# Optimization experiments

Hardware: AMD Instinct MI355X
Metric: run time of the kernel (lower is better)

The kernel has to match this reference:

```python
import jax, jax.numpy as jnp
from jax import lax
import numpy as np

O = 64      # out_channels (== in_channels == groups, depthwise)
P = 3       # prompt_len
K = 17      # prompt_size (large kernel size)
RANK = 4
# (small_kernel_size, pixel_unshuffle_scale, dilations) for prompt_size=17
CONFIGS = [(3, 4, (4, 5, 7)), (5, 2, (1,)), (9, 1, (2,))]


def conv2d(x, w, b=None, stride=1, padding=0, dilation=1, groups=1):
    out = lax.conv_general_dilated(
        x, w, (stride, stride), [(padding, padding)] * 2,
        rhs_dilation=(dilation, dilation), feature_group_count=groups,
        dimension_numbers=('NCHW', 'OIHW', 'NCHW'))
    return out if b is None else out + b[None, :, None, None]


def pixel_unshuffle(x, s):
    n, c, h, w = x.shape
    x = x.reshape(n, c, h // s, s, w // s, s)
    return x.transpose(0, 1, 3, 5, 2, 4).reshape(n, c * s * s, h // s, w // s)


def bilinear(x, oh, ow):
    # F.interpolate(mode='bilinear', align_corners=False); all uses downsample
    n, c, h, w = x.shape
    def coords(o, i):
        src = jnp.clip((jnp.arange(o, dtype=jnp.float32) + 0.5) * (i / o) - 0.5, 0.0, i - 1.0)
        i0 = jnp.floor(src).astype(jnp.int32)
        i1 = jnp.minimum(i0 + 1, i - 1)
        return i0, i1, src - i0.astype(jnp.float32)
    y0, y1, ty = coords(oh, h)
    x0, x1, tx = coords(ow, w)
    r0, r1 = x[:, :, y0], x[:, :, y1]
    top = r0[:, :, :, x0] * (1 - tx) + r0[:, :, :, x1] * tx
    bot = r1[:, :, :, x0] * (1 - tx) + r1[:, :, :, x1] * tx
    ty = ty[:, None]
    return top * (1 - ty) + bot * ty


def zero_interleave(k, d):
    # conv_transpose2d with 1x1 ones kernel, stride d == insert d-1 zeros
    o, c, ks, _ = k.shape
    e = d * (ks - 1) + 1
    return jnp.zeros((o, c, e, e), k.dtype).at[:, :, ::d, ::d].set(k)


def _branch(weight0, k_size, scale, dils, dw_w, dw_b, w1, b1, w2, b2, dilw, merged):
    w = weight0
    if scale > 1:
        ph = (-K) % scale
        w = jnp.pad(w, ((0, 0), (0, 0), (0, ph), (0, ph)))
        w = pixel_unshuffle(w, scale)
    h = conv2d(w, dw_w, dw_b, padding=1, groups=dw_w.shape[0])  # depthwise 3x3
    h = jax.nn.relu(conv2d(h, w1, b1))                          # 1x1 expand
    h = conv2d(h, w2, b2)                                       # 1x1 project
    h = bilinear(h, k_size, k_size)                             # (O, P*scale_or_P, k, k)
    for idx, d in enumerate(dils):
        dk = jnp.einsum('ochw,pc->ophw', h, dilw[idx])          # 1x1, no bias -> (O,P,k,k)
        eq = zero_interleave(dk, d)
        p = K // 2 - eq.shape[-1] // 2
        merged = merged + jnp.pad(eq, ((0, 0), (0, 0), (p, p), (p, p)))
    return merged


def _forward(x, A1, A2, A3, B1, B2, B3,
             dw_w3, dw_b3, w1_3, b1_3, w2_3, b2_3, dilw3,
             dw_w5, dw_b5, w1_5, b1_5, w2_5, b2_5, dilw5,
             dw_w9, dw_b9, w1_9, b1_9, w2_9, b2_9, dilw9):
    # low-rank reconstruction: (O,1,K,r) @ (O,1,r,K) -> (O,1,K,K), cat -> (O,P,K,K)
    weight0 = jnp.concatenate(
        [jnp.einsum('oikj,oijl->oikl', A, B) for A, B in ((A1, B1), (A2, B2), (A3, B3))],
        axis=1)
    merged = jnp.zeros_like(weight0)
    packs = [(dw_w3, dw_b3, w1_3, b1_3, w2_3, b2_3, dilw3),
             (dw_w5, dw_b5, w1_5, b1_5, w2_5, b2_5, dilw5),
             (dw_w9, dw_b9, w1_9, b1_9, w2_9, b2_9, dilw9)]
    for (k_size, scale, dils), pk in zip(CONFIGS, packs):
        merged = _branch(weight0, k_size, scale, dils, *pk, merged)
    w = merged.reshape(O * P, 1, K, K)
    return conv2d(x, w, padding=K // 2, groups=64)  # depthwise, 3 filters per channel


def setup_inputs() -> dict:
    key = jax.random.key(0)
    ks = iter(jax.random.split(key, 64))
    def rn(shape, s=0.05):
        return jax.random.normal(next(ks), shape, jnp.float32) * s
    inp = {'x': jax.random.normal(next(ks), (8, 64, 256, 256), jnp.float32)}
    for i in (1, 2, 3):
        inp[f'A{i}'] = rn((O, 1, K, RANK), 0.2)
        inp[f'B{i}'] = rn((O, 1, RANK, K), 0.2)
    # (pixel_unshuffle channels, hidden, mlp_out, n_dilations) per kernel size
    specs = {3: (48, 64, 12, 3), 5: (12, 48, 6, 1), 9: (3, 12, 3, 1)}
    for kk, (c, hid, out_c, nd) in specs.items():
        inp[f'dw_w{kk}'] = rn((c, 1, 3, 3))
        inp[f'dw_b{kk}'] = rn((c,))
        inp[f'w1_{kk}'] = rn((hid, c, 1, 1))
        inp[f'b1_{kk}'] = rn((hid,))
        inp[f'w2_{kk}'] = rn((out_c, hid, 1, 1))
        inp[f'b2_{kk}'] = rn((out_c,))
        inp[f'dilw{kk}'] = rn((nd, P, out_c))
    return inp


def reference(x, A1, A2, A3, B1, B2, B3,
              dw_w3, dw_b3, w1_3, b1_3, w2_3, b2_3, dilw3,
              dw_w5, dw_b5, w1_5, b1_5, w2_5, b2_5, dilw5,
              dw_w9, dw_b9, w1_9, b1_9, w2_9, b2_9, dilw9):
    return _forward(x, A1, A2, A3, B1, B2, B3,
                    dw_w3, dw_b3, w1_3, b1_3, w2_3, b2_3, dilw3,
                    dw_w5, dw_b5, w1_5, b1_5, w2_5, b2_5, dilw5,
                    dw_w9, dw_b9, w1_9, b1_9, w2_9, b2_9, dilw9)
```

## Files before the change

### kernel.cpp

```cpp
#include <hip/hip_runtime.h>
#include <cstddef>

typedef _Float16 h8 __attribute__((ext_vector_type(8)));
typedef float f4 __attribute__((ext_vector_type(4)));
typedef unsigned int uint32;

struct BranchP {
  int ksz, scale, CIN, HID, COUT, S, nd;
  int dils[3];
  const float *dw_w, *dw_b, *w1, *b1, *w2, *b2, *dilw;
};

__device__ void run_branch(int tid, const BranchP P,
                           const float* w0, float* merged,
                           float* bufA, float* bufB) {
  const int S = P.S, ksz = P.ksz, CIN = P.CIN, HID = P.HID, COUT = P.COUT;
  const int SS = S * S;
  for (int i = tid; i < CIN * SS; i += 256) {
    const int cc = i / SS, rem = i % SS, hh = rem / S, ww = rem % S;
    const int s2 = P.scale * P.scale;
    const int c = cc / s2, r2 = cc % s2, si = r2 / P.scale, sj = r2 % P.scale;
    const int sh = hh * P.scale + si, sw = ww * P.scale + sj;
    bufA[i] = (sh < 17 && sw < 17) ? w0[c * 289 + sh * 17 + sw] : 0.f;
  }
  __syncthreads();
  for (int i = tid; i < CIN * SS; i += 256) {
    const int ch = i / SS, rem = i % SS, y = rem / S, x = rem % S;
    float acc = P.dw_b[ch];
    for (int u = 0; u < 3; ++u)
      for (int v = 0; v < 3; ++v) {
        const int yy = y + u - 1, xx = x + v - 1;
        if (yy >= 0 && yy < S && xx >= 0 && xx < S)
          acc += bufA[ch * SS + yy * S + xx] * P.dw_w[ch * 9 + u * 3 + v];
      }
    bufB[i] = acc;
  }
  __syncthreads();
  for (int i = tid; i < HID * SS; i += 256) {
    const int ho = i / SS, rem = i % SS;
    float acc = P.b1[ho];
    for (int ci = 0; ci < CIN; ++ci) acc += bufB[ci * SS + rem] * P.w1[ho * CIN + ci];
    bufA[i] = fmaxf(acc, 0.f);
  }
  __syncthreads();
  for (int i = tid; i < COUT * SS; i += 256) {
    const int po = i / SS, rem = i % SS;
    float acc = P.b2[po];
    for (int ci = 0; ci < HID; ++ci) acc += bufA[ci * SS + rem] * P.w2[po * HID + ci];
    bufB[i] = acc;
  }
  __syncthreads();
  for (int i = tid; i < COUT * ksz * ksz; i += 256) {
    const int c = i / (ksz * ksz), rem = i % (ksz * ksz), oy = rem / ksz, ox = rem % ksz;
    const float ratio = (float)S / (float)ksz;
    float sy = fminf(fmaxf((oy + 0.5f) * ratio - 0.5f, 0.f), (float)(S - 1));
    float sx = fminf(fmaxf((ox + 0.5f) * ratio - 0.5f, 0.f), (float)(S - 1));
    const int y0 = (int)sy; const int y1 = min(y0 + 1, S - 1); const float ty = sy - (float)y0;
    const int x0 = (int)sx; const int x1 = min(x0 + 1, S - 1); const float tx = sx - (float)x0;
    const float* img = bufB + c * SS;
    const float top = img[y0 * S + x0] * (1.f - tx) + img[y0 * S + x1] * tx;
    const float bot = img[y1 * S + x0] * (1.f - tx) + img[y1 * S + x1] * tx;
    bufA[i] = top * (1.f - ty) + bot * ty;
  }
  __syncthreads();
  for (int di = 0; di < P.nd; ++di) {
    const int d = P.dils[di];
    const int e = d * (ksz - 1) + 1, pp = 8 - e / 2;
    for (int i = tid; i < 3 * ksz * ksz; i += 256) {
      const int p = i / (ksz * ksz), rem = i % (ksz * ksz), ih = rem / ksz, iw = rem % ksz;
      float acc = 0.f;
      for (int c2 = 0; c2 < COUT; ++c2)
        acc += bufA[c2 * ksz * ksz + rem] * P.dilw[(di * 3 + p) * COUT + c2];
      merged[p * 289 + (pp + d * ih) * 17 + (pp + d * iw)] += acc;
    }
  }
  __syncthreads();
}

#define KPAD 416
#define ACH (2 * 16 * KPAD)

__global__ __launch_bounds__(256) void prep_kernel(
    const float* __restrict__ A1, const float* __restrict__ B1,
    const float* __restrict__ A2, const float* __restrict__ B2,
    const float* __restrict__ A3, const float* __restrict__ B3,
    const float* __restrict__ dw_w3, const float* __restrict__ dw_b3,
    const float* __restrict__ w1_3, const float* __restrict__ b1_3,
    const float* __restrict__ w2_3, const float* __restrict__ b2_3,
    const float* __restrict__ dilw3,
    const float* __restrict__ dw_w5, const float* __restrict__ dw_b5,
    const float* __restrict__ w1_5, const float* __restrict__ b1_5,
    const float* __restrict__ w2_5, const float* __restrict__ b2_5,
    const float* __restrict__ dilw5,
    const float* __restrict__ dw_w9, const float* __restrict__ dw_b9,
    const float* __restrict__ w1_9, const float* __restrict__ b1_9,
    const float* __restrict__ w2_9, const float* __restrict__ b2_9,
    const float* __restrict__ dilw9,
    _Float16* __restrict__ wA) {
  const int o = blockIdx.x;
  const int tid = threadIdx.x;
  __shared__ float w0[3 * 289];
  __shared__ float merged[3 * 289];
  __shared__ float bufA[3888];
  __shared__ float bufB[3888];

  for (int i = tid; i < 3 * 289; i += 256) {
    const int c = i / 289, rem = i % 289, k = rem / 17, l = rem % 17;
    const float* A = (c == 0 ? A1 : (c == 1 ? A2 : A3)) + o * 68;
    const float* B = (c == 0 ? B1 : (c == 1 ? B2 : B3)) + o * 68;
    float s = 0.f;
    for (int r = 0; r < 4; ++r) s += A[k * 4 + r] * B[r * 17 + l];
    w0[i] = s;
    merged[i] = 0.f;
  }
  __syncthreads();

  {
    BranchP P{3, 4, 48, 64, 12, 5, 3, {4, 5, 7}, dw_w3, dw_b3, w1_3, b1_3, w2_3, b2_3, dilw3};
    run_branch(tid, P, w0, merged, bufA, bufB);
  }
  {
    BranchP P{5, 2, 12, 48, 6, 9, 1, {1, 0, 0}, dw_w5, dw_b5, w1_5, b1_5, w2_5, b2_5, dilw5};
    run_branch(tid, P, w0, merged, bufA, bufB);
  }
  {
    BranchP P{9, 1, 3, 12, 3, 17, 1, {2, 0, 0}, dw_w9, dw_b9, w1_9, b1_9, w2_9, b2_9, dilw9};
    run_branch(tid, P, w0, merged, bufA, bufB);
  }

  for (int i = tid; i < ACH; i += 256) {
    const int g = i / (16 * KPAD);
    const int m = (i / KPAD) % 16;
    const int k = i % KPAD;
    const int dxi = k / 24, r = k % 24;
    int pp, yo;
    if (g == 0) { pp = m & 1; yo = m >> 1; } else { pp = 2; yo = m; }
    const int dy = r - 8 - yo;
    float val = 0.f;
    if (!(g == 1 && m >= 8) && dy >= -8 && dy <= 8 && dxi <= 16)
      val = merged[pp * 289 + (dy + 8) * 17 + dxi];
    wA[(size_t)o * ACH + i] = (_Float16)val;
  }
}

__global__ __launch_bounds__(256) void conv_mfma_kernel(
    const float* __restrict__ xin, const _Float16* __restrict__ wA,
    float* __restrict__ out) {
  const int yg = blockIdx.x * 32;
  const int ch = blockIdx.y;
  const int n  = blockIdx.z;
  const int tid = threadIdx.x;

#define PITCH 56
  __shared__ __align__(16) _Float16 Xt[280 * PITCH];

  const float* xim = xin + ((size_t)(n * 64 + ch)) * 65536;

  const int lane = tid & 63;
  const int wv = tid >> 6;
  const int row = lane & 15;
  const int kg = lane >> 4;

  h8 a1[13], a2[13];
  {
    const _Float16* Ab = wA + (size_t)ch * ACH + row * KPAD;
    #pragma unroll
    for (int t = 0; t < 13; ++t) {
      const int k0 = t * 32 + kg * 8;
      a1[t] = __builtin_bit_cast(h8, *(const uint4*)(Ab + k0));
      a2[t] = __builtin_bit_cast(h8, *(const uint4*)(Ab + 16 * KPAD + k0));
    }
  }

  for (int i = tid; i < 6 * 280; i += 256) {
    const int rb = i / 280, c = i % 280;
    const int gx = c - 8;
    const bool cok = (gx >= 0 && gx < 256);
    float v[8];
    #pragma unroll
    for (int rr = 0; rr < 8; ++rr) {
      const int gy = yg - 8 + rb * 8 + rr;
      v[rr] = (cok && gy >= 0 && gy < 256) ? xim[gy * 256 + gx] : 0.f;
    }
    uint4 u;
    u.x = __builtin_bit_cast(uint32, __builtin_amdgcn_cvt_pkrtz(v[0], v[1]));
    u.y = __builtin_bit_cast(uint32, __builtin_amdgcn_cvt_pkrtz(v[2], v[3]));
    u.z = __builtin_bit_cast(uint32, __builtin_amdgcn_cvt_pkrtz(v[4], v[5]));
    u.w = __builtin_bit_cast(uint32, __builtin_amdgcn_cvt_pkrtz(v[6], v[7]));
    *(uint4*)&Xt[c * PITCH + rb * 8] = u;
  }
  __syncthreads();

  int boff[13];
  #pragma unroll
  for (int t = 0; t < 13; ++t) {
    const int k0 = t * 32 + kg * 8;
    const int dxi = k0 / 24, r0 = k0 - dxi * 24;
    boff[t] = (row + dxi) * PITCH + r0;
  }

  for (int pr = 0; pr < 8; ++pr) {
    const int g = pr >> 1, cp = pr & 1;
    const int j0a = (wv * 4 + cp * 2) * 16;
    const int ba = j0a * PITCH + 8 * g;
    const int bb = ba + 16 * PITCH;
    f4 c1a = {0.f, 0.f, 0.f, 0.f}, c2a = {0.f, 0.f, 0.f, 0.f};
    f4 c1b = {0.f, 0.f, 0.f, 0.f}, c2b = {0.f, 0.f, 0.f, 0.f};
    #pragma unroll
    for (int t = 0; t < 13; ++t) {
      const h8 vba = __builtin_bit_cast(h8, *(const uint4*)&Xt[ba + boff[t]]);
      const h8 vbb = __builtin_bit_cast(h8, *(const uint4*)&Xt[bb + boff[t]]);
      c1a = __builtin_amdgcn_mfma_f32_16x16x32_f16(a1[t], vba, c1a, 0, 0, 0);
      c1b = __builtin_amdgcn_mfma_f32_16x16x32_f16(a1[t], vbb, c1b, 0, 0, 0);
      c2a = __builtin_amdgcn_mfma_f32_16x16x32_f16(a2[t], vba, c2a, 0, 0, 0);
      c2b = __builtin_amdgcn_mfma_f32_16x16x32_f16(a2[t], vbb, c2b, 0, 0, 0);
    }
    const int ygg = yg + 8 * g;
    #pragma unroll
    for (int half = 0; half < 2; ++half) {
      const int gx = j0a + half * 16 + row;
      const f4 s1 = half ? c1b : c1a;
      const f4 s2 = half ? c2b : c2a;
      #pragma unroll
      for (int reg = 0; reg < 4; ++reg) {
        const int r = kg * 4 + reg;
        out[(((size_t)n * 192 + ch * 3 + (r & 1)) * 256 + (ygg + (r >> 1))) * 256 + gx] = s1[reg];
      }
      if (kg < 2) {
        #pragma unroll
        for (int reg = 0; reg < 4; ++reg) {
          const int r = kg * 4 + reg;
          out[(((size_t)n * 192 + ch * 3 + 2) * 256 + (ygg + r)) * 256 + gx] = s2[reg];
        }
      }
    }
  }
#undef PITCH
}

extern "C" void kernel_launch(void* const* d_in, const int* in_sizes, int n_in,
                              void* d_out, int out_size, void* d_ws, size_t ws_size,
                              hipStream_t stream) {
  const float* xin = (const float*)d_in[0];
  const float* A1 = (const float*)d_in[1];
  const float* B1 = (const float*)d_in[2];
  const float* A2 = (const float*)d_in[3];
  const float* B2 = (const float*)d_in[4];
  const float* A3 = (const float*)d_in[5];
  const float* B3 = (const float*)d_in[6];
  const float* dw_w3 = (const float*)d_in[7];
  const float* dw_b3 = (const float*)d_in[8];
  const float* w1_3 = (const float*)d_in[9];
  const float* b1_3 = (const float*)d_in[10];
  const float* w2_3 = (const float*)d_in[11];
  const float* b2_3 = (const float*)d_in[12];
  const float* dilw3 = (const float*)d_in[13];
  const float* dw_w5 = (const float*)d_in[14];
  const float* dw_b5 = (const float*)d_in[15];
  const float* w1_5 = (const float*)d_in[16];
  const float* b1_5 = (const float*)d_in[17];
  const float* w2_5 = (const float*)d_in[18];
  const float* b2_5 = (const float*)d_in[19];
  const float* dilw5 = (const float*)d_in[20];
  const float* dw_w9 = (const float*)d_in[21];
  const float* dw_b9 = (const float*)d_in[22];
  const float* w1_9 = (const float*)d_in[23];
  const float* b1_9 = (const float*)d_in[24];
  const float* w2_9 = (const float*)d_in[25];
  const float* b2_9 = (const float*)d_in[26];
  const float* dilw9 = (const float*)d_in[27];

  _Float16* wA = (_Float16*)d_ws;

  prep_kernel<<<64, 256, 0, stream>>>(
      A1, B1, A2, B2, A3, B3,
      dw_w3, dw_b3, w1_3, b1_3, w2_3, b2_3, dilw3,
      dw_w5, dw_b5, w1_5, b1_5, w2_5, b2_5, dilw5,
      dw_w9, dw_b9, w1_9, b1_9, w2_9, b2_9, dilw9,
      wA);

  dim3 grid(8, 64, 8);
  conv_mfma_kernel<<<grid, 256, 0, stream>>>(xin, wA, (float*)d_out);
}
```

Measured before the change: 207.5 us.

## Restructure MFMA loop to stream weights per k-step and remap blocks across XCDs

The conv kernel now keeps all 32 output accumulators (4 column tiles x 4 row groups, two weight halves) live and iterates once over the 13 k-steps, loading each weight fragment from global memory just in time with one-step prefetch instead of holding 26 weight vectors in registers. The grid is flattened to 1D with an index swizzle so that consecutive block IDs (which are dealt round-robin across XCDs) map to the same image and channel neighbourhood, improving L2 locality. A launch bound of 3 blocks per SM is added to cap register use. The risks are a larger accumulator footprint (128 VGPRs of accumulators) that could force spills under the new bound, and global weight loads now sitting inside the main loop.

```diff
diff --git a/kernel.cpp b/kernel.cpp
--- a/kernel.cpp
+++ b/kernel.cpp
@@ -143,12 +143,13 @@
   }
 }
 
-__global__ __launch_bounds__(256) void conv_mfma_kernel(
+__global__ __launch_bounds__(256, 3) void conv_mfma_kernel(
     const float* __restrict__ xin, const _Float16* __restrict__ wA,
     float* __restrict__ out) {
-  const int yg = blockIdx.x * 32;
-  const int ch = blockIdx.y;
-  const int n  = blockIdx.z;
+  const int wid = ((blockIdx.x & 7) << 9) + (blockIdx.x >> 3);
+  const int n   = wid >> 9;
+  const int ch  = (wid >> 3) & 63;
+  const int yg  = (wid & 7) * 32;
   const int tid = threadIdx.x;
 
 #define PITCH 56
@@ -160,17 +161,6 @@
   const int wv = tid >> 6;
   const int row = lane & 15;
   const int kg = lane >> 4;
-
-  h8 a1[13], a2[13];
-  {
-    const _Float16* Ab = wA + (size_t)ch * ACH + row * KPAD;
-    #pragma unroll
-    for (int t = 0; t < 13; ++t) {
-      const int k0 = t * 32 + kg * 8;
-      a1[t] = __builtin_bit_cast(h8, *(const uint4*)(Ab + k0));
-      a2[t] = __builtin_bit_cast(h8, *(const uint4*)(Ab + 16 * KPAD + k0));
-    }
-  }
 
   for (int i = tid; i < 6 * 280; i += 256) {
     const int rb = i / 280, c = i % 280;
@@ -191,50 +181,66 @@
   }
   __syncthreads();
 
-  int boff[13];
+  const _Float16* Abase = wA + (size_t)ch * ACH + row * KPAD + kg * 8;
+  const int wbase = (wv * 64) * PITCH;
+
+#define ALD(off) __builtin_bit_cast(h8, *(const uint4*)(Abase + (off)))
+
+  f4 c1[4][4], c2[4][4];
   #pragma unroll
+  for (int c = 0; c < 4; ++c)
+    #pragma unroll
+    for (int g = 0; g < 4; ++g) {
+      c1[c][g] = (f4){0.f, 0.f, 0.f, 0.f};
+      c2[c][g] = (f4){0.f, 0.f, 0.f, 0.f};
+    }
+
+  h8 p1 = ALD(0);
+  h8 p2 = ALD(16 * KPAD);
+
+  #pragma unroll 1
   for (int t = 0; t < 13; ++t) {
+    const h8 a1v = p1, a2v = p2;
+    if (t < 12) {
+      p1 = ALD((t + 1) * 32);
+      p2 = ALD(16 * KPAD + (t + 1) * 32);
+    }
     const int k0 = t * 32 + kg * 8;
     const int dxi = k0 / 24, r0 = k0 - dxi * 24;
-    boff[t] = (row + dxi) * PITCH + r0;
-  }
-
-  for (int pr = 0; pr < 8; ++pr) {
-    const int g = pr >> 1, cp = pr & 1;
-    const int j0a = (wv * 4 + cp * 2) * 16;
-    const int ba = j0a * PITCH + 8 * g;
-    const int bb = ba + 16 * PITCH;
-    f4 c1a = {0.f, 0.f, 0.f, 0.f}, c2a = {0.f, 0.f, 0.f, 0.f};
-    f4 c1b = {0.f, 0.f, 0.f, 0.f}, c2b = {0.f, 0.f, 0.f, 0.f};
-    #pragma unroll
-    for (int t = 0; t < 13; ++t) {
-      const h8 vba = __builtin_bit_cast(h8, *(const uint4*)&Xt[ba + boff[t]]);
-      const h8 vbb = __builtin_bit_cast(h8, *(const uint4*)&Xt[bb + boff[t]]);
-      c1a = __builtin_amdgcn_mfma_f32_16x16x32_f16(a1[t], vba, c1a, 0, 0, 0);
-      c1b = __builtin_amdgcn_mfma_f32_16x16x32_f16(a1[t], vbb, c1b, 0, 0, 0);
-      c2a = __builtin_amdgcn_mfma_f32_16x16x32_f16(a2[t], vba, c2a, 0, 0, 0);
-      c2b = __builtin_amdgcn_mfma_f32_16x16x32_f16(a2[t], vbb, c2b, 0, 0, 0);
-    }
-    const int ygg = yg + 8 * g;
-    #pragma unroll
-    for (int half = 0; half < 2; ++half) {
-      const int gx = j0a + half * 16 + row;
-      const f4 s1 = half ? c1b : c1a;
-      const f4 s2 = half ? c2b : c2a;
+    const int bo = wbase + (row + dxi) * PITCH + r0;
+    #pragma unroll
+    for (int c = 0; c < 4; ++c) {
+      #pragma unroll
+      for (int g = 0; g < 4; ++g) {
+        const h8 b = __builtin_bit_cast(
+            h8, *(const uint4*)&Xt[bo + c * 16 * PITCH + g * 8]);
+        c1[c][g] = __builtin_amdgcn_mfma_f32_16x16x32_f16(a1v, b, c1[c][g], 0, 0, 0);
+        c2[c][g] = __builtin_amdgcn_mfma_f32_16x16x32_f16(a2v, b, c2[c][g], 0, 0, 0);
+      }
+    }
+  }
+
+  #pragma unroll
+  for (int c = 0; c < 4; ++c) {
+    const int gx = (wv * 4 + c) * 16 + row;
+    #pragma unroll
+    for (int g = 0; g < 4; ++g) {
+      const int ygg = yg + 8 * g;
       #pragma unroll
       for (int reg = 0; reg < 4; ++reg) {
         const int r = kg * 4 + reg;
-        out[(((size_t)n * 192 + ch * 3 + (r & 1)) * 256 + (ygg + (r >> 1))) * 256 + gx] = s1[reg];
+        out[(((size_t)n * 192 + ch * 3 + (r & 1)) * 256 + (ygg + (r >> 1))) * 256 + gx] = c1[c][g][reg];
       }
       if (kg < 2) {
         #pragma unroll
         for (int reg = 0; reg < 4; ++reg) {
           const int r = kg * 4 + reg;
-          out[(((size_t)n * 192 + ch * 3 + 2) * 256 + (ygg + r)) * 256 + gx] = s2[reg];
+          out[(((size_t)n * 192 + ch * 3 + 2) * 256 + (ygg + r)) * 256 + gx] = c2[c][g][reg];
         }
       }
     }
   }
+#undef ALD
 #undef PITCH
 }
 
@@ -279,6 +285,5 @@
       dw_w9, dw_b9, w1_9, b1_9, w2_9, b2_9, dilw9,
       wA);
 
-  dim3 grid(8, 64, 8);
-  conv_mfma_kernel<<<grid, 256, 0, stream>>>(xin, wA, (float*)d_out);
-}
+  conv_mfma_kernel<<<dim3(4096), 256, 0, stream>>>(xin, wA, (float*)d_out);
+}
```

After: 276.5 us. 1.33x slower.
